# Optimization experiments

Hardware: AMD Instinct MI355X
Metric: run time of the kernel (lower is better)

The kernel has to match this reference:

```python
import jax, jax.numpy as jnp
import numpy as np

TOKENS, IN_F, OUT_F = 8192, 4096, 4096

def setup_inputs() -> dict:
    key = jax.random.key(0)
    k1, k2, k3, k4 = jax.random.split(key, 4)
    x = jax.random.randint(k1, (TOKENS, IN_F), -128, 128, dtype=jnp.int32).astype(jnp.int8)
    weight = jax.random.randint(k2, (OUT_F, IN_F), -128, 128, dtype=jnp.int32).astype(jnp.int8)
    # per-output-channel static dequant scale (small positive values, as for int8 quant)
    dequant_scale = (jax.random.uniform(k3, (OUT_F,), dtype=jnp.float32) * 0.01 + 1e-4)
    bias = (jax.random.normal(k4, (OUT_F,), dtype=jnp.float32) * 0.02).astype(jnp.float16)
    return {"x": x, "weight": weight, "dequant_scale": dequant_scale, "bias": bias}

def reference(x, weight, dequant_scale, bias):
    acc = jnp.matmul(x.astype(jnp.int32), weight.T.astype(jnp.int32))
    # fused epilogue: per-channel dequant + bias add, cast to fp16 output
    out = (acc.astype(jnp.float32) * dequant_scale[None, :]
           + bias.astype(jnp.float32)[None, :]).astype(jnp.float16)
    # module's forward returns (output, bias)
    return (out, bias)
```

## Files before the change

### kernel.cpp

```cpp
#include <hip/hip_runtime.h>
#include <hip/hip_fp16.h>

#define TOKENS 8192
#define IN_F   4096
#define OUT_F  4096
#define NK64   (IN_F / 64)

#define REG    16384
#define BUFSZ  (2 * REG)
typedef __attribute__((ext_vector_type(4))) int i32x4;

__global__ void prep_kernel(const int4* __restrict__ xs, const int4* __restrict__ ws,
                            const float* __restrict__ bias,
                            int4* __restrict__ xp, int4* __restrict__ wp,
                            float* __restrict__ out_tail) {
    const int NX = TOKENS * IN_F / 16;
    const int NW = OUT_F * IN_F / 16;
    const int gid = blockIdx.x * blockDim.x + threadIdx.x;
    const int stride = gridDim.x * blockDim.x;
    for (int i = gid; i < NX + NW; i += stride) {
        const int4* s; int4* d; int j;
        if (i < NX) { s = xs; d = xp; j = i; }
        else        { s = ws; d = wp; j = i - NX; }
        int4 a = s[4 * j + 0];
        int4 b = s[4 * j + 1];
        int4 c = s[4 * j + 2];
        int4 e = s[4 * j + 3];
        int4 o;
        o.x = (int)((a.x & 0xffu) | ((a.y & 0xffu) << 8) | ((a.z & 0xffu) << 16) | ((a.w & 0xffu) << 24));
        o.y = (int)((b.x & 0xffu) | ((b.y & 0xffu) << 8) | ((b.z & 0xffu) << 16) | ((b.w & 0xffu) << 24));
        o.z = (int)((c.x & 0xffu) | ((c.y & 0xffu) << 8) | ((c.z & 0xffu) << 16) | ((c.w & 0xffu) << 24));
        o.w = (int)((e.x & 0xffu) | ((e.y & 0xffu) << 8) | ((e.z & 0xffu) << 16) | ((e.w & 0xffu) << 24));
        d[j] = o;
    }
    if (gid < OUT_F) out_tail[gid] = bias[gid];
}

__global__ __launch_bounds__(512, 2) void gemm_i8_kernel(
    const char* __restrict__ A,
    const char* __restrict__ B,
    const float* __restrict__ scale,
    const float* __restrict__ bias,
    float* __restrict__ out)
{
    __shared__ char lds[4 * BUFSZ];

    const int tid  = threadIdx.x;
    const int wid  = tid >> 6;
    const int lane = tid & 63;
    const int wm   = wid >> 2;
    const int wn   = wid & 3;

    const int bid   = blockIdx.x;
    const int xcd   = bid & 7;
    const int j9    = bid >> 3;
    const int rect  = (j9 >> 5) * 8 + xcd;
    const int jj    = j9 & 31;
    const int tm    = (rect & 3) * 8 + (jj & 7);
    const int tn    = (rect >> 2) * 4 + (jj >> 3);

    const char* ag = A + (size_t)(tm * 256) * IN_F;
    const char* bg = B + (size_t)(tn * 256) * IN_F;

    const size_t gsub = (size_t)((tid >> 6) * 16 + (tid & 15)) * IN_F + (((tid >> 4) & 3) << 4);
    const int    ldst = tid * 16;

#define STAGE(r, t)                                                                        \
    do {                                                                                   \
        _Pragma("unroll")                                                                  \
        for (int i = 0; i < 2; ++i) {                                                      \
            size_t go = (size_t)(i * 128) * IN_F + gsub + (size_t)(t) * 64;                \
            __builtin_amdgcn_global_load_lds(                                              \
                (const __attribute__((address_space(1))) void*)(ag + go),                  \
                (__attribute__((address_space(3))) void*)(&lds[(r) * BUFSZ +               \
                                                              i * 8192 + ldst]),           \
                16, 0, 0);                                                                 \
            __builtin_amdgcn_global_load_lds(                                              \
                (const __attribute__((address_space(1))) void*)(bg + go),                  \
                (__attribute__((address_space(3))) void*)(&lds[(r) * BUFSZ + REG +         \
                                                              i * 8192 + ldst]),           \
                16, 0, 0);                                                                 \
        }                                                                                  \
    } while (0)

    const int aoff = wm * 8 * 1024 + lane * 16;
    const int boff = REG + wn * 4 * 1024 + lane * 16;

    i32x4 acc[8][4];
#pragma unroll
    for (int m = 0; m < 8; ++m)
#pragma unroll
        for (int n = 0; n < 4; ++n)
            acc[m][n] = (i32x4){0, 0, 0, 0};

    STAGE(0, 0);
    STAGE(1, 1);
    STAGE(2, 2);

#define TILE(t, VM, DOSTAGE)                                                               \
    do {                                                                                   \
        asm volatile("s_waitcnt vmcnt(" #VM ")" ::: "memory");                             \
        __builtin_amdgcn_s_barrier();                                                      \
        __builtin_amdgcn_sched_barrier(0);                                                 \
        const char* Lr = &lds[((t) & 3) * BUFSZ];                                          \
        i32x4 af[8], bf[4];                                                                \
        _Pragma("unroll")                                                                  \
        for (int n = 0; n < 4; ++n)                                                        \
            bf[n] = *(const i32x4*)(Lr + boff + n * 1024);                                 \
        _Pragma("unroll")                                                                  \
        for (int m = 0; m < 8; ++m)                                                        \
            af[m] = *(const i32x4*)(Lr + aoff + m * 1024);                                 \
        if (DOSTAGE) STAGE(((t) + 3) & 3, (t) + 3);                                        \
        __builtin_amdgcn_s_setprio(1);                                                     \
        _Pragma("unroll")                                                                  \
        for (int m = 0; m < 8; ++m)                                                        \
            _Pragma("unroll")                                                              \
            for (int n = 0; n < 4; ++n)                                                    \
                acc[m][n] = __builtin_amdgcn_mfma_i32_16x16x64_i8(                         \
                    af[m], bf[n], acc[m][n], 0, 0, 0);                                     \
        __builtin_amdgcn_s_setprio(0);                                                     \
    } while (0)

#pragma unroll 1
    for (int t = 0; t <= NK64 - 4; ++t) TILE(t, 8, 1);
    TILE(NK64 - 3, 8, 0);
    TILE(NK64 - 2, 4, 0);
    TILE(NK64 - 1, 0, 0);

    const int col  = tn * 256 + wn * 64 + (lane & 15);
    const int row0 = tm * 256 + wm * 128 + ((lane >> 4) << 2);
    float sc[4], bi[4];
#pragma unroll
    for (int n = 0; n < 4; ++n) {
        sc[n] = scale[col + n * 16];
        bi[n] = bias[col + n * 16];
    }
#pragma unroll
    for (int m = 0; m < 8; ++m)
#pragma unroll
        for (int n = 0; n < 4; ++n)
#pragma unroll
            for (int r = 0; r < 4; ++r) {
                float v = (float)acc[m][n][r] * sc[n] + bi[n];
                out[(size_t)(row0 + m * 16 + r) * OUT_F + col + n * 16] =
                    (float)__float2half_rn(v);
            }
#undef STAGE
#undef TILE
}

extern "C" void kernel_launch(void* const* d_in, const int* in_sizes, int n_in,
                              void* d_out, int out_size, void* d_ws, size_t ws_size,
                              hipStream_t stream) {
    const int*   x_i32 = (const int*)d_in[0];
    const int*   w_i32 = (const int*)d_in[1];
    const float* scale = (const float*)d_in[2];
    const float* bias  = (const float*)d_in[3];
    float*       out   = (float*)d_out;

    char* xp = (char*)d_ws;
    char* wp = xp + (size_t)TOKENS * IN_F;

    prep_kernel<<<3072, 256, 0, stream>>>((const int4*)x_i32, (const int4*)w_i32, bias,
                                          (int4*)xp, (int4*)wp, out + (size_t)TOKENS * OUT_F);

    gemm_i8_kernel<<<(TOKENS / 256) * (OUT_F / 256), 512, 0, stream>>>(xp, wp, scale, bias, out);
}
```

Measured before the change: 204.0 us.

## Pre-tile int8 operands in prep kernel so GEMM loads are contiguous

The prep kernel now writes the packed int8 A and B into a blocked layout that matches the LDS staging order: one contiguous 16 KB chunk per 256-row tile per 64-wide K step. The GEMM then issues fully linear global_load_lds reads instead of strided row gathers. This aims to improve coalescing and TLB/cache behaviour in the main loop. In exchange, the prep kernel does scattered reads from the int32 inputs, which may slow the conversion pass.

```diff
diff --git a/kernel.cpp b/kernel.cpp
--- a/kernel.cpp
+++ b/kernel.cpp
@@ -10,28 +10,35 @@
 #define BUFSZ  (2 * REG)
 typedef __attribute__((ext_vector_type(4))) int i32x4;
 
-__global__ void prep_kernel(const int4* __restrict__ xs, const int4* __restrict__ ws,
+__global__ void prep_kernel(const int* __restrict__ xs, const int* __restrict__ ws,
                             const float* __restrict__ bias,
                             int4* __restrict__ xp, int4* __restrict__ wp,
                             float* __restrict__ out_tail) {
-    const int NX = TOKENS * IN_F / 16;
-    const int NW = OUT_F * IN_F / 16;
+    const int NA = (TOKENS / 256) * 64 * 1024;
+    const int NB = (OUT_F  / 256) * 64 * 1024;
     const int gid = blockIdx.x * blockDim.x + threadIdx.x;
     const int stride = gridDim.x * blockDim.x;
-    for (int i = gid; i < NX + NW; i += stride) {
-        const int4* s; int4* d; int j;
-        if (i < NX) { s = xs; d = xp; j = i; }
-        else        { s = ws; d = wp; j = i - NX; }
-        int4 a = s[4 * j + 0];
-        int4 b = s[4 * j + 1];
-        int4 c = s[4 * j + 2];
-        int4 e = s[4 * j + 3];
+    for (int s = gid; s < NA + NB; s += stride) {
+        const int* src; int4* dst; int t2;
+        if (s < NA) { src = xs; dst = xp; t2 = s; }
+        else        { src = ws; dst = wp; t2 = s - NA; }
+        const int slot = t2 & 1023;
+        const int blk  = t2 >> 10;
+        const int f    = slot >> 6;
+        const int l    = slot & 63;
+        const int row  = (blk >> 6) * 256 + f * 16 + (l & 15);
+        const int k0   = (blk & 63) * 64 + ((l >> 4) << 4);
+        const int* p   = src + (size_t)row * IN_F + k0;
+        int4 a = *(const int4*)(p + 0);
+        int4 b = *(const int4*)(p + 4);
+        int4 c = *(const int4*)(p + 8);
+        int4 e = *(const int4*)(p + 12);
         int4 o;
         o.x = (int)((a.x & 0xffu) | ((a.y & 0xffu) << 8) | ((a.z & 0xffu) << 16) | ((a.w & 0xffu) << 24));
         o.y = (int)((b.x & 0xffu) | ((b.y & 0xffu) << 8) | ((b.z & 0xffu) << 16) | ((b.w & 0xffu) << 24));
         o.z = (int)((c.x & 0xffu) | ((c.y & 0xffu) << 8) | ((c.z & 0xffu) << 16) | ((c.w & 0xffu) << 24));
         o.w = (int)((e.x & 0xffu) | ((e.y & 0xffu) << 8) | ((e.z & 0xffu) << 16) | ((e.w & 0xffu) << 24));
-        d[j] = o;
+        dst[t2] = o;
     }
     if (gid < OUT_F) out_tail[gid] = bias[gid];
 }
@@ -59,17 +66,15 @@
     const int tm    = (rect & 3) * 8 + (jj & 7);
     const int tn    = (rect >> 2) * 4 + (jj >> 3);
 
-    const char* ag = A + (size_t)(tm * 256) * IN_F;
-    const char* bg = B + (size_t)(tn * 256) * IN_F;
-
-    const size_t gsub = (size_t)((tid >> 6) * 16 + (tid & 15)) * IN_F + (((tid >> 4) & 3) << 4);
-    const int    ldst = tid * 16;
+    const char* ag = A + (size_t)tm * (64 * 16384);
+    const char* bg = B + (size_t)tn * (64 * 16384);
+    const int   ldst = tid * 16;
 
 #define STAGE(r, t)                                                                        \
     do {                                                                                   \
         _Pragma("unroll")                                                                  \
         for (int i = 0; i < 2; ++i) {                                                      \
-            size_t go = (size_t)(i * 128) * IN_F + gsub + (size_t)(t) * 64;                \
+            size_t go = (size_t)(t) * 16384 + i * 8192 + ldst;                             \
             __builtin_amdgcn_global_load_lds(                                              \
                 (const __attribute__((address_space(1))) void*)(ag + go),                  \
                 (__attribute__((address_space(3))) void*)(&lds[(r) * BUFSZ +               \
@@ -161,7 +166,7 @@
     char* xp = (char*)d_ws;
     char* wp = xp + (size_t)TOKENS * IN_F;
 
-    prep_kernel<<<3072, 256, 0, stream>>>((const int4*)x_i32, (const int4*)w_i32, bias,
+    prep_kernel<<<3072, 256, 0, stream>>>(x_i32, w_i32, bias,
                                           (int4*)xp, (int4*)wp, out + (size_t)TOKENS * OUT_F);
 
     gemm_i8_kernel<<<(TOKENS / 256) * (OUT_F / 256), 512, 0, stream>>>(xp, wp, scale, bias, out);
```

New measurement: 183.9 us. 1.11x faster.
